# Kernel optimization log

Hardware: AMD Instinct MI355X
Metric: run time of the kernel (lower is better)

## Reference

```python
import jax, jax.numpy as jnp
import numpy as np

N, E = 10000, 320000
C_IN, C_OUT = 256, 128
EPS = 1e-5


def _p(key, shape, scale=0.02):
    return (jax.random.normal(key, shape, dtype=jnp.float32) * scale)


def setup_inputs() -> dict:
    key = jax.random.key(0)
    ks = jax.random.split(key, 16)
    inp = {
        "x": jax.random.normal(ks[0], (N, C_IN), dtype=jnp.float32),
        "edge_index": jax.random.randint(ks[1], (2, E), 0, N, dtype=jnp.int64),
        # GCNConv weights (stored [in, out] so forward is x @ W)
        "W1": _p(ks[2], (C_IN, C_OUT)), "b1": jnp.zeros((C_OUT,), jnp.float32),
        "W2": _p(ks[3], (C_OUT, C_OUT)), "b2": jnp.zeros((C_OUT,), jnp.float32),
        # LayerNorms
        "ln1_g": jnp.ones((C_OUT,), jnp.float32), "ln1_b": jnp.zeros((C_OUT,), jnp.float32),
        "ln2_g": jnp.ones((C_OUT,), jnp.float32), "ln2_b": jnp.zeros((C_OUT,), jnp.float32),
        # Attention QKV
        "Wq": _p(ks[4], (C_OUT, C_OUT)), "bq": jnp.zeros((C_OUT,), jnp.float32),
        "Wk": _p(ks[5], (C_OUT, C_OUT)), "bk": jnp.zeros((C_OUT,), jnp.float32),
        "Wv": _p(ks[6], (C_OUT, C_OUT)), "bv": jnp.zeros((C_OUT,), jnp.float32),
        # shortcut Linear (in_channels != out_channels)
        "Ws": _p(ks[7], (C_IN, C_OUT)), "bs": jnp.zeros((C_OUT,), jnp.float32),
    }
    return inp


def _gcn_conv(x, W, b, src, dst, n_nodes):
    # PyG GCNConv: h = x W; add self loops; sym-normalized scatter aggregation.
    h = x @ W  # [N, out]
    loop = jnp.arange(n_nodes, dtype=src.dtype)
    s = jnp.concatenate([src, loop])
    d = jnp.concatenate([dst, loop])
    deg = jax.ops.segment_sum(jnp.ones_like(d, dtype=h.dtype), d, num_segments=n_nodes)
    dis = jnp.where(deg > 0, jax.lax.rsqrt(deg), 0.0)  # deg^-1/2
    norm = dis[s] * dis[d]  # [E+N]
    agg = jax.ops.segment_sum(h[s] * norm[:, None], d, num_segments=n_nodes)
    return agg + b


def _layer_norm(x, g, b):
    mu = jnp.mean(x, axis=-1, keepdims=True)
    var = jnp.var(x, axis=-1, keepdims=True)
    return (x - mu) * jax.lax.rsqrt(var + EPS) * g + b


def reference(x, edge_index, W1, b1, W2, b2, ln1_g, ln1_b, ln2_g, ln2_b,
              Wq, bq, Wk, bk, Wv, bv, Ws, bs):
    src, dst = edge_index[0], edge_index[1]
    n = x.shape[0]
    identity = x @ Ws + bs
    out = _gcn_conv(x, W1, b1, src, dst, n)
    out = jax.nn.silu(_layer_norm(out, ln1_g, ln1_b))  # dropout = identity (eval)
    out = _gcn_conv(out, W2, b2, src, dst, n)
    out = _layer_norm(out, ln2_g, ln2_b)
    # dense self-attention over all nodes
    q = out @ Wq + bq
    k = out @ Wk + bk
    v = out @ Wv + bv
    scale = np.sqrt(out.shape[-1]).astype(np.float32)
    attn = jax.nn.softmax(q @ k.T / scale, axis=-1)  # [N, N]
    out = attn @ v + out
    return jax.nn.silu(out + identity)
```

## Files before the change

kernel.cpp:

```cpp
#include <hip/hip_runtime.h>
#include <hip/hip_bf16.h>

typedef unsigned short u16;
typedef unsigned int u32;
typedef __bf16 bf16x8 __attribute__((ext_vector_type(8)));
typedef float f32x4 __attribute__((ext_vector_type(4)));

#define MFMA16(a, b, c) __builtin_amdgcn_mfma_f32_16x16x32_bf16(a, b, c, 0, 0, 0)

static __device__ __forceinline__ u16 f2b(float f) {
  u32 u = __float_as_uint(f);
  return (u16)((u + 0x7FFFu + ((u >> 16) & 1u)) >> 16);
}
static __device__ __forceinline__ float blo(u32 u) { return __uint_as_float(u << 16); }
static __device__ __forceinline__ float bhi(u32 u) { return __uint_as_float(u & 0xffff0000u); }

static __device__ __forceinline__ void async_copy16(void* lds, const void* gp) {
  __builtin_amdgcn_global_load_lds(
      (const __attribute__((address_space(1))) unsigned int*)gp,
      (__attribute__((address_space(3))) unsigned int*)lds, 16, 0, 0);
}

__global__ void prep_kernel(const int* __restrict__ dst, int* __restrict__ degi, int E,
                            const float* __restrict__ x, u16* __restrict__ xb, int n4,
                            const float* __restrict__ W1, const float* __restrict__ Ws,
                            const float* __restrict__ W2, const float* __restrict__ Wq,
                            const float* __restrict__ Wk, const float* __restrict__ Wv,
                            u16* __restrict__ wout) {
  int t = blockIdx.x * 256 + threadIdx.x;
  if (t < E) { atomicAdd(&degi[dst[t]], 1); return; }
  int t2 = t - E;
  if (t2 < n4) {
    float4 v = *(const float4*)&x[t2 * 4];
    ushort4 o;
    o.x = f2b(v.x); o.y = f2b(v.y); o.z = f2b(v.z); o.w = f2b(v.w);
    *(ushort4*)&xb[t2 * 4] = o;
    return;
  }
  int u = t2 - n4;
  if (u >= 131072) return;
  const float* src; int K, base, loc;
  if (u < 65536) {
    if (u < 32768) { src = W1; base = 0; } else { src = Ws; base = 32768; }
    loc = u - base; K = 256;
  } else {
    int seg = (u - 65536) >> 14;
    src = (seg == 0) ? W2 : (seg == 1) ? Wq : (seg == 2) ? Wk : Wv;
    base = 65536 + seg * 16384; loc = u & 16383; K = 128;
  }
  int k = loc >> 7, c = loc & 127;
  wout[base + c * K + k] = f2b(src[loc]);
}

__global__ void dis_start_kernel(const int* __restrict__ degi, float* __restrict__ d,
                                 int* __restrict__ startb, int* __restrict__ counter, int N) {
  int i = blockIdx.x * 256 + threadIdx.x;
  int lane = threadIdx.x & 63;
  int dg = (i < N) ? degi[i] : 0;
  if (i < N) d[i] = rsqrtf((float)dg + 1.0f);
  int x = dg;
#pragma unroll
  for (int ofs = 1; ofs < 64; ofs <<= 1) {
    int y = __shfl_up(x, ofs, 64);
    if (lane >= ofs) x += y;
  }
  int waveTotal = __shfl(x, 63, 64);
  int base = 0;
  if (lane == 63) base = atomicAdd(counter, waveTotal);
  base = __shfl(base, 63, 64);
  if (i < N) startb[i] = base + x - dg;
}

__global__ void fill_kernel(const int* __restrict__ src, const int* __restrict__ dst,
                            const int* __restrict__ startb, int* __restrict__ cursor,
                            int* __restrict__ adj, int E) {
  int e = blockIdx.x * 256 + threadIdx.x;
  if (e < E) {
    int d = dst[e];
    int p = atomicAdd(&cursor[d], 1);
    adj[startb[d] + p] = src[e];
  }
}

__global__ __launch_bounds__(64) void bgemm_dual(
    const u16* __restrict__ A, const u16* __restrict__ Wa, const u16* __restrict__ Wb,
    const float* __restrict__ bsb, u16* __restrict__ outa, float* __restrict__ outb, int M)
{
  int lane = threadIdx.x;
  int col = lane & 15, quad = lane >> 4;
  int row0 = blockIdx.x * 16;
  int cb = blockIdx.y * 64;
  int ar = row0 + col; if (ar > M - 1) ar = M - 1;
  const u16* ap = A + (size_t)ar * 256 + quad * 8;
  f32x4 Oa[4], Ob[4];
#pragma unroll
  for (int i = 0; i < 4; i++) {
    Oa[i][0] = 0.f; Oa[i][1] = 0.f; Oa[i][2] = 0.f; Oa[i][3] = 0.f;
    Ob[i] = Oa[i];
  }
#pragma unroll
  for (int k0 = 0; k0 < 256; k0 += 32) {
    bf16x8 aA = *(const bf16x8*)(ap + k0);
#pragma unroll
    for (int nb = 0; nb < 4; nb++) {
      size_t wofs = (size_t)(cb + nb * 16 + col) * 256 + k0 + quad * 8;
      Oa[nb] = MFMA16(aA, *(const bf16x8*)(Wa + wofs), Oa[nb]);
      Ob[nb] = MFMA16(aA, *(const bf16x8*)(Wb + wofs), Ob[nb]);
    }
  }
#pragma unroll
  for (int nb = 0; nb < 4; nb++) {
    int ch = cb + nb * 16 + col;
    float bv = bsb[ch];
#pragma unroll
    for (int r = 0; r < 4; r++) {
      int row = row0 + quad * 4 + r;
      if (row >= M) continue;
      outa[(size_t)row * 128 + ch] = f2b(Oa[nb][r]);
      outb[(size_t)row * 128 + ch] = Ob[nb][r] + bv;
    }
  }
}

__global__ __launch_bounds__(64) void bgemm_single(
    const u16* __restrict__ A, const u16* __restrict__ Wt, u16* __restrict__ outa, int M)
{
  int lane = threadIdx.x;
  int col = lane & 15, quad = lane >> 4;
  int row0 = blockIdx.x * 16;
  int cb = blockIdx.y * 64;
  int ar = row0 + col; if (ar > M - 1) ar = M - 1;
  const u16* ap = A + (size_t)ar * 128 + quad * 8;
  f32x4 O[4];
#pragma unroll
  for (int i = 0; i < 4; i++) { O[i][0] = 0.f; O[i][1] = 0.f; O[i][2] = 0.f; O[i][3] = 0.f; }
#pragma unroll
  for (int k0 = 0; k0 < 128; k0 += 32) {
    bf16x8 aA = *(const bf16x8*)(ap + k0);
#pragma unroll
    for (int nb = 0; nb < 4; nb++) {
      O[nb] = MFMA16(aA, *(const bf16x8*)(Wt + (size_t)(cb + nb * 16 + col) * 128 + k0 + quad * 8), O[nb]);
    }
  }
#pragma unroll
  for (int nb = 0; nb < 4; nb++) {
    int ch = cb + nb * 16 + col;
#pragma unroll
    for (int r = 0; r < 4; r++) {
      int row = row0 + quad * 4 + r;
      if (row >= M) continue;
      outa[(size_t)row * 128 + ch] = f2b(O[nb][r]);
    }
  }
}

__global__ __launch_bounds__(64) void bgemm_qkv(
    const u16* __restrict__ A, const u16* __restrict__ Wqt, const u16* __restrict__ Wkt,
    const u16* __restrict__ Wvt, const float* __restrict__ bq, const float* __restrict__ bk,
    const float* __restrict__ bv, u16* __restrict__ q_out, u16* __restrict__ k_out,
    u16* __restrict__ v_out, int M, int NP, float qscale)
{
  int lane = threadIdx.x;
  int col = lane & 15, quad = lane >> 4;
  int row0 = blockIdx.x * 16;
  int cb = blockIdx.y * 64;
  int ar = row0 + col; if (ar > M - 1) ar = M - 1;
  const u16* ap = A + (size_t)ar * 128 + quad * 8;
  f32x4 Oq[4], Ok[4], Ov[4];
#pragma unroll
  for (int i = 0; i < 4; i++) {
    Oq[i][0] = 0.f; Oq[i][1] = 0.f; Oq[i][2] = 0.f; Oq[i][3] = 0.f;
    Ok[i] = Oq[i]; Ov[i] = Oq[i];
  }
#pragma unroll
  for (int k0 = 0; k0 < 128; k0 += 32) {
    bf16x8 aA = *(const bf16x8*)(ap + k0);
#pragma unroll
    for (int nb = 0; nb < 4; nb++) {
      size_t wofs = (size_t)(cb + nb * 16 + col) * 128 + k0 + quad * 8;
      Oq[nb] = MFMA16(aA, *(const bf16x8*)(Wqt + wofs), Oq[nb]);
      Ok[nb] = MFMA16(aA, *(const bf16x8*)(Wkt + wofs), Ok[nb]);
      Ov[nb] = MFMA16(aA, *(const bf16x8*)(Wvt + wofs), Ov[nb]);
    }
  }
#pragma unroll
  for (int nb = 0; nb < 4; nb++) {
    int ch = cb + nb * 16 + col;
    float bqv = bq[ch], bkv = bk[ch], bvv = bv[ch];
#pragma unroll
    for (int r = 0; r < 4; r++) {
      int row = row0 + quad * 4 + r;
      if (row >= M) continue;
      q_out[(size_t)row * 128 + ch] = f2b((Oq[nb][r] + bqv) * qscale);
      k_out[(size_t)row * 128 + ch] = f2b(Ok[nb][r] + bkv);
      v_out[(size_t)ch * NP + row] = f2b(Ov[nb][r] + bvv);
    }
  }
}

__global__ __launch_bounds__(256) void gather_ln(
    const u16* __restrict__ h, const float* __restrict__ dis,
    const int* __restrict__ adj, const int* __restrict__ startb, const int* __restrict__ degi,
    const float* __restrict__ bias, const float* __restrict__ g, const float* __restrict__ beta,
    float* __restrict__ out, u16* __restrict__ outb, int N, int do_silu)
{
  int row = blockIdx.x * 4 + (threadIdx.x >> 6);
  int lane = threadIdx.x & 63;
  if (row >= N) return;
  int st = startb[row], dg = degi[row];
  int c2 = lane * 2;
  float v0 = 0.f, v1 = 0.f;
  for (int base = 0; base < dg; base += 64) {
    int nb = min(64, dg - base);
    int myadj = 0; float mydis = 0.f;
    if (lane < nb) { myadj = adj[st + base + lane]; mydis = dis[myadj]; }
    int jj = 0;
    for (; jj + 8 <= nb; jj += 8) {
      int s0 = __shfl(myadj, jj),     s1 = __shfl(myadj, jj + 1);
      int s2 = __shfl(myadj, jj + 2), s3 = __shfl(myadj, jj + 3);
      int s4 = __shfl(myadj, jj + 4), s5 = __shfl(myadj, jj + 5);
      int s6 = __shfl(myadj, jj + 6), s7 = __shfl(myadj, jj + 7);
      float w0 = __shfl(mydis, jj),     w1 = __shfl(mydis, jj + 1);
      float w2 = __shfl(mydis, jj + 2), w3 = __shfl(mydis, jj + 3);
      float w4 = __shfl(mydis, jj + 4), w5 = __shfl(mydis, jj + 5);
      float w6 = __shfl(mydis, jj + 6), w7 = __shfl(mydis, jj + 7);
      u32 a0 = *(const u32*)&h[(size_t)s0 * 128 + c2];
      u32 a1 = *(const u32*)&h[(size_t)s1 * 128 + c2];
      u32 a2 = *(const u32*)&h[(size_t)s2 * 128 + c2];
      u32 a3 = *(const u32*)&h[(size_t)s3 * 128 + c2];
      u32 a4 = *(const u32*)&h[(size_t)s4 * 128 + c2];
      u32 a5 = *(const u32*)&h[(size_t)s5 * 128 + c2];
      u32 a6 = *(const u32*)&h[(size_t)s6 * 128 + c2];
      u32 a7 = *(const u32*)&h[(size_t)s7 * 128 + c2];
      v0 += w0 * blo(a0); v1 += w0 * bhi(a0);
      v0 += w1 * blo(a1); v1 += w1 * bhi(a1);
      v0 += w2 * blo(a2); v1 += w2 * bhi(a2);
      v0 += w3 * blo(a3); v1 += w3 * bhi(a3);
      v0 += w4 * blo(a4); v1 += w4 * bhi(a4);
      v0 += w5 * blo(a5); v1 += w5 * bhi(a5);
      v0 += w6 * blo(a6); v1 += w6 * bhi(a6);
      v0 += w7 * blo(a7); v1 += w7 * bhi(a7);
    }
    for (; jj < nb; jj++) {
      int s = __shfl(myadj, jj);
      float wv = __shfl(mydis, jj);
      u32 a = *(const u32*)&h[(size_t)s * 128 + c2];
      v0 += wv * blo(a); v1 += wv * bhi(a);
    }
  }
  float dd = dis[row];
  u32 aself = *(const u32*)&h[(size_t)row * 128 + c2];
  v0 = (v0 + dd * blo(aself)) * dd + bias[c2];
  v1 = (v1 + dd * bhi(aself)) * dd + bias[c2 + 1];
  float s = v0 + v1;
#pragma unroll
  for (int d = 32; d > 0; d >>= 1) s += __shfl_xor(s, d, 64);
  float mu = s * (1.0f / 128.0f);
  float d0 = v0 - mu, d1 = v1 - mu;
  float q = d0 * d0 + d1 * d1;
#pragma unroll
  for (int d = 32; d > 0; d >>= 1) q += __shfl_xor(q, d, 64);
  float rstd = rsqrtf(q * (1.0f / 128.0f) + 1e-5f);
  float o0 = d0 * rstd * g[c2]     + beta[c2];
  float o1 = d1 * rstd * g[c2 + 1] + beta[c2 + 1];
  if (do_silu) {
    o0 = o0 / (1.f + __expf(-o0));
    o1 = o1 / (1.f + __expf(-o1));
  }
  size_t base = (size_t)row * 128;
  *(float2*)&out[base + c2] = make_float2(o0, o1);
  u32 pk = (u32)f2b(o0) | ((u32)f2b(o1) << 16);
  *(u32*)&outb[base + c2] = pk;
}

__global__ __launch_bounds__(256, 3) void flash_part(
    const u16* __restrict__ qb, const u16* __restrict__ kb, const u16* __restrict__ vt,
    u16* __restrict__ Opart, float* __restrict__ lpart,
    int N, int NP, int CHUNK)
{
  __shared__ __align__(16) u16 Kl[2][32 * 128];
  __shared__ __align__(16) u16 Vl[2][128 * 32];
  __shared__ __align__(16) u16 Pl[4][32][40];
  int tid = threadIdx.x;
  int w = tid >> 6, lane = tid & 63;
  int col = lane & 15, quad = lane >> 4;
  int h8 = col & 7;
  int ks = blockIdx.y;
  int kstart = ks * CHUNK;
  int qbase = blockIdx.x * 128 + w * 32;

  bf16x8 aQ[2][4];
#pragma unroll
  for (int rg = 0; rg < 2; rg++) {
    int qr = qbase + rg * 16 + col; if (qr > N - 1) qr = N - 1;
    const u16* qp = qb + (size_t)qr * 128 + quad * 8;
    aQ[rg][0] = *(const bf16x8*)(qp);
    aQ[rg][1] = *(const bf16x8*)(qp + 32);
    aQ[rg][2] = *(const bf16x8*)(qp + 64);
    aQ[rg][3] = *(const bf16x8*)(qp + 96);
  }

  f32x4 O[2][8];
#pragma unroll
  for (int rg = 0; rg < 2; rg++)
#pragma unroll
    for (int i = 0; i < 8; i++) { O[rg][i][0] = 0.f; O[rg][i][1] = 0.f; O[rg][i][2] = 0.f; O[rg][i][3] = 0.f; }
  float lr[2][4] = {{0.f, 0.f, 0.f, 0.f}, {0.f, 0.f, 0.f, 0.f}};

  int l16 = lane >> 4, c16 = lane & 15;
  int vch = lane >> 2, vc4 = lane & 3;

  auto stage = [&](int buf, int k0) {
#pragma unroll
    for (int i = 0; i < 2; i++) {
      int rl = w * 8 + i * 4 + l16;
      int cg = c16 ^ (rl & 7);
      async_copy16(&Kl[buf][(w * 8 + i * 4) * 128], kb + (size_t)(k0 + rl) * 128 + cg * 8);
    }
#pragma unroll
    for (int i = 0; i < 2; i++) {
      int ch = w * 32 + i * 16 + vch;
      int cg = vc4 ^ ((ch >> 1) & 3);
      async_copy16(&Vl[buf][(w * 32 + i * 16) * 32], vt + (size_t)ch * NP + k0 + cg * 8);
    }
  };

  int KT = (min(CHUNK, NP - kstart)) >> 5;
  stage(0, kstart);

  for (int kt = 0; kt < KT; kt++) {
    int buf = kt & 1;
    int k0 = kstart + (kt << 5);
    asm volatile("s_waitcnt vmcnt(0)\n\ts_barrier" ::: "memory");
    if (kt + 1 < KT) stage(buf ^ 1, k0 + 32);

    const u16* Kb = &Kl[buf][0];
    const u16* Vb = &Vl[buf][0];
    bool edge = (k0 + 32 > N);
#pragma unroll
    for (int g = 0; g < 2; g++) {
      const u16* kr = Kb + (g * 16 + col) * 128;
      bf16x8 kf0 = *(const bf16x8*)(kr + (((0 + quad) ^ h8) << 3));
      bf16x8 kf1 = *(const bf16x8*)(kr + (((4 + quad) ^ h8) << 3));
      bf16x8 kf2 = *(const bf16x8*)(kr + (((8 + quad) ^ h8) << 3));
      bf16x8 kf3 = *(const bf16x8*)(kr + (((12 + quad) ^ h8) << 3));
      f32x4 s0; s0[0] = 0.f; s0[1] = 0.f; s0[2] = 0.f; s0[3] = 0.f;
      f32x4 s1 = s0;
      s0 = MFMA16(aQ[0][0], kf0, s0); s1 = MFMA16(aQ[1][0], kf0, s1);
      s0 = MFMA16(aQ[0][1], kf1, s0); s1 = MFMA16(aQ[1][1], kf1, s1);
      s0 = MFMA16(aQ[0][2], kf2, s0); s1 = MFMA16(aQ[1][2], kf2, s1);
      s0 = MFMA16(aQ[0][3], kf3, s0); s1 = MFMA16(aQ[1][3], kf3, s1);
      if (edge && (k0 + g * 16 + col >= N)) {
        s0[0] = -1e30f; s0[1] = -1e30f; s0[2] = -1e30f; s0[3] = -1e30f;
        s1 = s0;
      }
#pragma unroll
      for (int r = 0; r < 4; r++) {
        float p0 = __expf(s0[r]);
        float p1 = __expf(s1[r]);
        lr[0][r] += p0;
        lr[1][r] += p1;
        Pl[w][quad * 4 + r][g * 16 + col]      = (u16)(__float_as_uint(p0) >> 16);
        Pl[w][16 + quad * 4 + r][g * 16 + col] = (u16)(__float_as_uint(p1) >> 16);
      }
    }
    asm volatile("s_waitcnt lgkmcnt(0)" ::: "memory");
    bf16x8 aP0 = *(const bf16x8*)&Pl[w][col][quad * 8];
    bf16x8 aP1 = *(const bf16x8*)&Pl[w][16 + col][quad * 8];
#pragma unroll
    for (int nb = 0; nb < 8; nb++) {
      int ch = nb * 16 + col;
      const u16* vr = Vb + ch * 32;
      bf16x8 vf = *(const bf16x8*)(vr + ((quad ^ ((ch >> 1) & 3)) << 3));
      O[0][nb] = MFMA16(aP0, vf, O[0][nb]);
      O[1][nb] = MFMA16(aP1, vf, O[1][nb]);
    }
  }

#pragma unroll
  for (int d = 1; d < 16; d <<= 1) {
#pragma unroll
    for (int rg = 0; rg < 2; rg++)
#pragma unroll
      for (int r = 0; r < 4; r++) lr[rg][r] += __shfl_xor(lr[rg][r], d, 64);
  }

#pragma unroll
  for (int rg = 0; rg < 2; rg++) {
#pragma unroll
    for (int nb = 0; nb < 8; nb++) {
      int ch = nb * 16 + col;
#pragma unroll
      for (int r = 0; r < 4; r++) {
        int row = qbase + rg * 16 + quad * 4 + r;
        if (row < N)
          Opart[((size_t)ks * NP + row) * 128 + ch] = f2b(O[rg][nb][r]);
      }
    }
  }
  if (col == 0) {
#pragma unroll
    for (int rg = 0; rg < 2; rg++)
#pragma unroll
      for (int r = 0; r < 4; r++) {
        int row = qbase + rg * 16 + quad * 4 + r;
        if (row < N) lpart[(size_t)ks * NP + row] = lr[rg][r];
      }
  }
}

__global__ __launch_bounds__(256) void attn_combine(
    const u16* __restrict__ Opart, const float* __restrict__ lpart,
    const float* __restrict__ out2, const float* __restrict__ ident, float* __restrict__ out,
    int N, int NP, int S)
{
  int row = blockIdx.x * 4 + (threadIdx.x >> 6);
  int c2 = (threadIdx.x & 63) * 2;
  if (row >= N) return;
  float num0 = 0.f, num1 = 0.f, den = 0.f;
  for (int u = 0; u < S; u++) {
    u32 b = *(const u32*)&Opart[((size_t)u * NP + row) * 128 + c2];
    num0 += blo(b); num1 += bhi(b);
    den += lpart[(size_t)u * NP + row];
  }
  size_t idx = (size_t)row * 128 + c2;
  float rinv = 1.0f / den;
  float2 o2 = *(const float2*)&out2[idx];
  float2 id = *(const float2*)&ident[idx];
  float v0 = num0 * rinv + o2.x + id.x;
  float v1 = num1 * rinv + o2.y + id.y;
  v0 = v0 / (1.f + __expf(-v0));
  v1 = v1 / (1.f + __expf(-v1));
  *(float2*)&out[idx] = make_float2(v0, v1);
}

extern "C" void kernel_launch(void* const* d_in, const int* in_sizes, int n_in,
                              void* d_out, int out_size, void* d_ws, size_t ws_size,
                              hipStream_t stream) {
  const float* x   = (const float*)d_in[0];
  const int*   ei  = (const int*)d_in[1];
  const float* W1  = (const float*)d_in[2];
  const float* b1  = (const float*)d_in[3];
  const float* W2  = (const float*)d_in[4];
  const float* b2  = (const float*)d_in[5];
  const float* g1  = (const float*)d_in[6];
  const float* be1 = (const float*)d_in[7];
  const float* g2  = (const float*)d_in[8];
  const float* be2 = (const float*)d_in[9];
  const float* Wq  = (const float*)d_in[10];
  const float* bq  = (const float*)d_in[11];
  const float* Wk  = (const float*)d_in[12];
  const float* bk  = (const float*)d_in[13];
  const float* Wv  = (const float*)d_in[14];
  const float* bv  = (const float*)d_in[15];
  const float* Wsw = (const float*)d_in[16];
  const float* bs  = (const float*)d_in[17];

  const int CIN = 256, C = 128;
  int N = in_sizes[0] / CIN;
  int E = in_sizes[1] / 2;
  int NP = (N + 63) & ~63;
  const int* src = ei;
  const int* dstp = ei + E;

  const int S = 12;
  int tiles = NP / 64;
  int CHUNK = ((tiles + S - 1) / S) * 64;

  char* w = (char*)d_ws;
  size_t off = 0;
  auto alloc = [&](size_t bytes) -> void* {
    void* p = w + off;
    off = (off + bytes + 255) & ~(size_t)255;
    return p;
  };
  int*   degi   = (int*)alloc((size_t)N * 4);
  int*   cursor = (int*)alloc((size_t)N * 4);
  int*   counter= (int*)alloc(256);
  size_t zlen   = off;
  float* disb   = (float*)alloc((size_t)N * 4);
  int*   startb = (int*)alloc((size_t)N * 4);
  int*   adj    = (int*)alloc((size_t)E * 4);
  u16*   h      = (u16*)alloc((size_t)N * C * 2);
  float* ident  = (float*)alloc((size_t)N * C * 4);
  float* cur    = (float*)alloc((size_t)N * C * 4);
  u16*   xb     = (u16*)alloc((size_t)N * CIN * 2);
  u16*   curb   = (u16*)alloc((size_t)N * C * 2);
  u16*   wt     = (u16*)alloc((size_t)131072 * 2);
  u16*   qbb    = (u16*)alloc((size_t)N * C * 2);
  u16*   kbb    = (u16*)alloc((size_t)NP * C * 2);
  u16*   vt     = (u16*)alloc((size_t)C * NP * 2);
  u16*   Opart  = (u16*)alloc((size_t)S * NP * C * 2);
  float* lpart  = (float*)alloc((size_t)S * NP * 4);

  u16* wt1 = wt;
  u16* wts = wt + 32768;
  u16* wt2 = wt + 65536;
  u16* wtq = wt + 81920;
  u16* wtk = wt + 98304;
  u16* wtv = wt + 114688;

  hipMemsetAsync(degi, 0, zlen, stream);

  int n4 = N * CIN / 4;
  int ptot = E + n4 + 131072;
  prep_kernel<<<(ptot + 255) / 256, 256, 0, stream>>>(dstp, degi, E, x, xb, n4,
                                                      W1, Wsw, W2, Wq, Wk, Wv, wt);
  int gN = (N + 255) / 256, gE = (E + 255) / 256;
  dis_start_kernel<<<gN, 256, 0, stream>>>(degi, disb, startb, counter, N);
  fill_kernel<<<gE, 256, 0, stream>>>(src, dstp, startb, cursor, adj, E);

  dim3 gbg((N + 15) / 16, 2);
  bgemm_dual<<<gbg, 64, 0, stream>>>(xb, wt1, wts, bs, h, ident, N);
  gather_ln<<<(N + 3) / 4, 256, 0, stream>>>(h, disb, adj, startb, degi, b1, g1, be1, cur, curb, N, 1);
  bgemm_single<<<gbg, 64, 0, stream>>>(curb, wt2, h, N);
  gather_ln<<<(N + 3) / 4, 256, 0, stream>>>(h, disb, adj, startb, degi, b2, g2, be2, cur, curb, N, 0);

  const float qscale = 0.08838834764831845f;
  bgemm_qkv<<<gbg, 64, 0, stream>>>(curb, wtq, wtk, wtv, bq, bk, bv, qbb, kbb, vt, N, NP, qscale);

  dim3 fg((N + 127) / 128, S);
  flash_part<<<fg, 256, 0, stream>>>(qbb, kbb, vt, Opart, lpart, N, NP, CHUNK);
  attn_combine<<<(N + 3) / 4, 256, 0, stream>>>(Opart, lpart, cur, ident,
                                                (float*)d_out, N, NP, S);
}
```

Baseline: 295.8 us.

## Fuse gather+LayerNorm with following GEMMs and keep softmax probabilities in registers

Merges each graph-aggregation+LayerNorm pass with the next small GEMM (W2, and QKV) through an LDS tile, removing two kernel launches and the intermediate bf16 round trips. The flash attention kernel now computes S^T by swapping MFMA operands, so P can be moved between lanes with ds_bpermute instead of a per-wave LDS buffer. It also writes packed Opart rows and uses row sums reduced by cross-lane shuffles. The split count S drops from 12 to 8 and partial buffers are padded to 128 rows. Fused gather blocks now process 16 rows serially across 4 waves, which may reduce latency hiding in the gather phase.

Result: no change. 294.0 us (-0.6%).

```diff
diff --git a/kernel.cpp b/kernel.cpp
--- a/kernel.cpp
+++ b/kernel.cpp
@@ -14,6 +14,12 @@
 }
 static __device__ __forceinline__ float blo(u32 u) { return __uint_as_float(u << 16); }
 static __device__ __forceinline__ float bhi(u32 u) { return __uint_as_float(u & 0xffff0000u); }
+static __device__ __forceinline__ u32 packtrunc(float a, float b) {
+  return (__float_as_uint(a) >> 16) | (__float_as_uint(b) & 0xffff0000u);
+}
+static __device__ __forceinline__ bf16x8 mk8(u32 a, u32 b, u32 c, u32 d) {
+  union { u32 u[4]; bf16x8 v; } t; t.u[0] = a; t.u[1] = b; t.u[2] = c; t.u[3] = d; return t.v;
+}
 
 static __device__ __forceinline__ void async_copy16(void* lds, const void* gp) {
   __builtin_amdgcn_global_load_lds(
@@ -122,165 +128,177 @@
   }
 }
 
-__global__ __launch_bounds__(64) void bgemm_single(
-    const u16* __restrict__ A, const u16* __restrict__ Wt, u16* __restrict__ outa, int M)
-{
-  int lane = threadIdx.x;
-  int col = lane & 15, quad = lane >> 4;
-  int row0 = blockIdx.x * 16;
-  int cb = blockIdx.y * 64;
-  int ar = row0 + col; if (ar > M - 1) ar = M - 1;
-  const u16* ap = A + (size_t)ar * 128 + quad * 8;
-  f32x4 O[4];
-#pragma unroll
-  for (int i = 0; i < 4; i++) { O[i][0] = 0.f; O[i][1] = 0.f; O[i][2] = 0.f; O[i][3] = 0.f; }
-#pragma unroll
-  for (int k0 = 0; k0 < 128; k0 += 32) {
-    bf16x8 aA = *(const bf16x8*)(ap + k0);
-#pragma unroll
-    for (int nb = 0; nb < 4; nb++) {
-      O[nb] = MFMA16(aA, *(const bf16x8*)(Wt + (size_t)(cb + nb * 16 + col) * 128 + k0 + quad * 8), O[nb]);
-    }
-  }
-#pragma unroll
-  for (int nb = 0; nb < 4; nb++) {
-    int ch = cb + nb * 16 + col;
-#pragma unroll
-    for (int r = 0; r < 4; r++) {
-      int row = row0 + quad * 4 + r;
-      if (row >= M) continue;
-      outa[(size_t)row * 128 + ch] = f2b(O[nb][r]);
-    }
-  }
-}
-
-__global__ __launch_bounds__(64) void bgemm_qkv(
-    const u16* __restrict__ A, const u16* __restrict__ Wqt, const u16* __restrict__ Wkt,
-    const u16* __restrict__ Wvt, const float* __restrict__ bq, const float* __restrict__ bk,
-    const float* __restrict__ bv, u16* __restrict__ q_out, u16* __restrict__ k_out,
-    u16* __restrict__ v_out, int M, int NP, float qscale)
-{
-  int lane = threadIdx.x;
-  int col = lane & 15, quad = lane >> 4;
-  int row0 = blockIdx.x * 16;
-  int cb = blockIdx.y * 64;
-  int ar = row0 + col; if (ar > M - 1) ar = M - 1;
-  const u16* ap = A + (size_t)ar * 128 + quad * 8;
-  f32x4 Oq[4], Ok[4], Ov[4];
-#pragma unroll
-  for (int i = 0; i < 4; i++) {
-    Oq[i][0] = 0.f; Oq[i][1] = 0.f; Oq[i][2] = 0.f; Oq[i][3] = 0.f;
-    Ok[i] = Oq[i]; Ov[i] = Oq[i];
-  }
-#pragma unroll
-  for (int k0 = 0; k0 < 128; k0 += 32) {
-    bf16x8 aA = *(const bf16x8*)(ap + k0);
-#pragma unroll
-    for (int nb = 0; nb < 4; nb++) {
-      size_t wofs = (size_t)(cb + nb * 16 + col) * 128 + k0 + quad * 8;
-      Oq[nb] = MFMA16(aA, *(const bf16x8*)(Wqt + wofs), Oq[nb]);
-      Ok[nb] = MFMA16(aA, *(const bf16x8*)(Wkt + wofs), Ok[nb]);
-      Ov[nb] = MFMA16(aA, *(const bf16x8*)(Wvt + wofs), Ov[nb]);
-    }
-  }
-#pragma unroll
-  for (int nb = 0; nb < 4; nb++) {
-    int ch = cb + nb * 16 + col;
-    float bqv = bq[ch], bkv = bk[ch], bvv = bv[ch];
-#pragma unroll
-    for (int r = 0; r < 4; r++) {
-      int row = row0 + quad * 4 + r;
-      if (row >= M) continue;
-      q_out[(size_t)row * 128 + ch] = f2b((Oq[nb][r] + bqv) * qscale);
-      k_out[(size_t)row * 128 + ch] = f2b(Ok[nb][r] + bkv);
-      v_out[(size_t)ch * NP + row] = f2b(Ov[nb][r] + bvv);
-    }
-  }
-}
-
-__global__ __launch_bounds__(256) void gather_ln(
+static __device__ __forceinline__ void gather_rows_to_lds(
     const u16* __restrict__ h, const float* __restrict__ dis,
     const int* __restrict__ adj, const int* __restrict__ startb, const int* __restrict__ degi,
     const float* __restrict__ bias, const float* __restrict__ g, const float* __restrict__ beta,
-    float* __restrict__ out, u16* __restrict__ outb, int N, int do_silu)
+    u16* Ao, float* curOut, int row0, int N, int do_silu)
 {
-  int row = blockIdx.x * 4 + (threadIdx.x >> 6);
+  int w = threadIdx.x >> 6, lane = threadIdx.x & 63;
+  int c2 = lane * 2;
+  for (int rr = 0; rr < 4; rr++) {
+    int rl = w * 4 + rr;
+    int row = row0 + rl;
+    float o0 = 0.f, o1 = 0.f;
+    if (row < N) {
+      int st = startb[row], dg = degi[row];
+      float v0 = 0.f, v1 = 0.f;
+      for (int base = 0; base < dg; base += 64) {
+        int nb = min(64, dg - base);
+        int myadj = 0; float mydis = 0.f;
+        if (lane < nb) { myadj = adj[st + base + lane]; mydis = dis[myadj]; }
+        int jj = 0;
+        for (; jj + 8 <= nb; jj += 8) {
+          int s0 = __shfl(myadj, jj),     s1 = __shfl(myadj, jj + 1);
+          int s2 = __shfl(myadj, jj + 2), s3 = __shfl(myadj, jj + 3);
+          int s4 = __shfl(myadj, jj + 4), s5 = __shfl(myadj, jj + 5);
+          int s6 = __shfl(myadj, jj + 6), s7 = __shfl(myadj, jj + 7);
+          float w0 = __shfl(mydis, jj),     w1 = __shfl(mydis, jj + 1);
+          float w2 = __shfl(mydis, jj + 2), w3 = __shfl(mydis, jj + 3);
+          float w4 = __shfl(mydis, jj + 4), w5 = __shfl(mydis, jj + 5);
+          float w6 = __shfl(mydis, jj + 6), w7 = __shfl(mydis, jj + 7);
+          u32 a0 = *(const u32*)&h[(size_t)s0 * 128 + c2];
+          u32 a1 = *(const u32*)&h[(size_t)s1 * 128 + c2];
+          u32 a2 = *(const u32*)&h[(size_t)s2 * 128 + c2];
+          u32 a3 = *(const u32*)&h[(size_t)s3 * 128 + c2];
+          u32 a4 = *(const u32*)&h[(size_t)s4 * 128 + c2];
+          u32 a5 = *(const u32*)&h[(size_t)s5 * 128 + c2];
+          u32 a6 = *(const u32*)&h[(size_t)s6 * 128 + c2];
+          u32 a7 = *(const u32*)&h[(size_t)s7 * 128 + c2];
+          v0 += w0 * blo(a0); v1 += w0 * bhi(a0);
+          v0 += w1 * blo(a1); v1 += w1 * bhi(a1);
+          v0 += w2 * blo(a2); v1 += w2 * bhi(a2);
+          v0 += w3 * blo(a3); v1 += w3 * bhi(a3);
+          v0 += w4 * blo(a4); v1 += w4 * bhi(a4);
+          v0 += w5 * blo(a5); v1 += w5 * bhi(a5);
+          v0 += w6 * blo(a6); v1 += w6 * bhi(a6);
+          v0 += w7 * blo(a7); v1 += w7 * bhi(a7);
+        }
+        for (; jj < nb; jj++) {
+          int s = __shfl(myadj, jj);
+          float wv = __shfl(mydis, jj);
+          u32 a = *(const u32*)&h[(size_t)s * 128 + c2];
+          v0 += wv * blo(a); v1 += wv * bhi(a);
+        }
+      }
+      float dd = dis[row];
+      u32 aself = *(const u32*)&h[(size_t)row * 128 + c2];
+      v0 = (v0 + dd * blo(aself)) * dd + bias[c2];
+      v1 = (v1 + dd * bhi(aself)) * dd + bias[c2 + 1];
+      float s = v0 + v1;
+#pragma unroll
+      for (int d = 32; d > 0; d >>= 1) s += __shfl_xor(s, d, 64);
+      float mu = s * (1.0f / 128.0f);
+      float d0 = v0 - mu, d1 = v1 - mu;
+      float q = d0 * d0 + d1 * d1;
+#pragma unroll
+      for (int d = 32; d > 0; d >>= 1) q += __shfl_xor(q, d, 64);
+      float rstd = rsqrtf(q * (1.0f / 128.0f) + 1e-5f);
+      o0 = d0 * rstd * g[c2]     + beta[c2];
+      o1 = d1 * rstd * g[c2 + 1] + beta[c2 + 1];
+      if (do_silu) {
+        o0 = o0 / (1.f + __expf(-o0));
+        o1 = o1 / (1.f + __expf(-o1));
+      }
+      if (curOut) *(float2*)&curOut[(size_t)row * 128 + c2] = make_float2(o0, o1);
+    }
+    *(u32*)&Ao[rl * 136 + c2] = (u32)f2b(o0) | ((u32)f2b(o1) << 16);
+  }
+}
+
+__global__ __launch_bounds__(256) void gather_gemm1(
+    const u16* __restrict__ h, const float* __restrict__ dis,
+    const int* __restrict__ adj, const int* __restrict__ startb, const int* __restrict__ degi,
+    const float* __restrict__ b1, const float* __restrict__ g1, const float* __restrict__ be1,
+    const u16* __restrict__ W2t, u16* __restrict__ h2, int N)
+{
+  __shared__ __align__(16) u16 Ao[16 * 136];
+  int row0 = blockIdx.x * 16;
+  gather_rows_to_lds(h, dis, adj, startb, degi, b1, g1, be1, Ao, nullptr, row0, N, 1);
+  __syncthreads();
   int lane = threadIdx.x & 63;
-  if (row >= N) return;
-  int st = startb[row], dg = degi[row];
-  int c2 = lane * 2;
-  float v0 = 0.f, v1 = 0.f;
-  for (int base = 0; base < dg; base += 64) {
-    int nb = min(64, dg - base);
-    int myadj = 0; float mydis = 0.f;
-    if (lane < nb) { myadj = adj[st + base + lane]; mydis = dis[myadj]; }
-    int jj = 0;
-    for (; jj + 8 <= nb; jj += 8) {
-      int s0 = __shfl(myadj, jj),     s1 = __shfl(myadj, jj + 1);
-      int s2 = __shfl(myadj, jj + 2), s3 = __shfl(myadj, jj + 3);
-      int s4 = __shfl(myadj, jj + 4), s5 = __shfl(myadj, jj + 5);
-      int s6 = __shfl(myadj, jj + 6), s7 = __shfl(myadj, jj + 7);
-      float w0 = __shfl(mydis, jj),     w1 = __shfl(mydis, jj + 1);
-      float w2 = __shfl(mydis, jj + 2), w3 = __shfl(mydis, jj + 3);
-      float w4 = __shfl(mydis, jj + 4), w5 = __shfl(mydis, jj + 5);
-      float w6 = __shfl(mydis, jj + 6), w7 = __shfl(mydis, jj + 7);
-      u32 a0 = *(const u32*)&h[(size_t)s0 * 128 + c2];
-      u32 a1 = *(const u32*)&h[(size_t)s1 * 128 + c2];
-      u32 a2 = *(const u32*)&h[(size_t)s2 * 128 + c2];
-      u32 a3 = *(const u32*)&h[(size_t)s3 * 128 + c2];
-      u32 a4 = *(const u32*)&h[(size_t)s4 * 128 + c2];
-      u32 a5 = *(const u32*)&h[(size_t)s5 * 128 + c2];
-      u32 a6 = *(const u32*)&h[(size_t)s6 * 128 + c2];
-      u32 a7 = *(const u32*)&h[(size_t)s7 * 128 + c2];
-      v0 += w0 * blo(a0); v1 += w0 * bhi(a0);
-      v0 += w1 * blo(a1); v1 += w1 * bhi(a1);
-      v0 += w2 * blo(a2); v1 += w2 * bhi(a2);
-      v0 += w3 * blo(a3); v1 += w3 * bhi(a3);
-      v0 += w4 * blo(a4); v1 += w4 * bhi(a4);
-      v0 += w5 * blo(a5); v1 += w5 * bhi(a5);
-      v0 += w6 * blo(a6); v1 += w6 * bhi(a6);
-      v0 += w7 * blo(a7); v1 += w7 * bhi(a7);
-    }
-    for (; jj < nb; jj++) {
-      int s = __shfl(myadj, jj);
-      float wv = __shfl(mydis, jj);
-      u32 a = *(const u32*)&h[(size_t)s * 128 + c2];
-      v0 += wv * blo(a); v1 += wv * bhi(a);
-    }
-  }
-  float dd = dis[row];
-  u32 aself = *(const u32*)&h[(size_t)row * 128 + c2];
-  v0 = (v0 + dd * blo(aself)) * dd + bias[c2];
-  v1 = (v1 + dd * bhi(aself)) * dd + bias[c2 + 1];
-  float s = v0 + v1;
-#pragma unroll
-  for (int d = 32; d > 0; d >>= 1) s += __shfl_xor(s, d, 64);
-  float mu = s * (1.0f / 128.0f);
-  float d0 = v0 - mu, d1 = v1 - mu;
-  float q = d0 * d0 + d1 * d1;
-#pragma unroll
-  for (int d = 32; d > 0; d >>= 1) q += __shfl_xor(q, d, 64);
-  float rstd = rsqrtf(q * (1.0f / 128.0f) + 1e-5f);
-  float o0 = d0 * rstd * g[c2]     + beta[c2];
-  float o1 = d1 * rstd * g[c2 + 1] + beta[c2 + 1];
-  if (do_silu) {
-    o0 = o0 / (1.f + __expf(-o0));
-    o1 = o1 / (1.f + __expf(-o1));
-  }
-  size_t base = (size_t)row * 128;
-  *(float2*)&out[base + c2] = make_float2(o0, o1);
-  u32 pk = (u32)f2b(o0) | ((u32)f2b(o1) << 16);
-  *(u32*)&outb[base + c2] = pk;
+  int w = threadIdx.x >> 6;
+  int col = lane & 15, quad = lane >> 4;
+  int nb0 = w * 2;
+  f32x4 acc[2];
+#pragma unroll
+  for (int t = 0; t < 2; t++) { acc[t][0] = 0.f; acc[t][1] = 0.f; acc[t][2] = 0.f; acc[t][3] = 0.f; }
+#pragma unroll
+  for (int ks = 0; ks < 4; ks++) {
+    bf16x8 aA = *(const bf16x8*)&Ao[col * 136 + ks * 32 + quad * 8];
+#pragma unroll
+    for (int t = 0; t < 2; t++) {
+      const u16* bp = W2t + (size_t)((nb0 + t) * 16 + col) * 128 + ks * 32 + quad * 8;
+      acc[t] = MFMA16(aA, *(const bf16x8*)bp, acc[t]);
+    }
+  }
+#pragma unroll
+  for (int t = 0; t < 2; t++) {
+    int ch = (nb0 + t) * 16 + col;
+#pragma unroll
+    for (int r = 0; r < 4; r++) {
+      int row = row0 + quad * 4 + r;
+      if (row < N) h2[(size_t)row * 128 + ch] = f2b(acc[t][r]);
+    }
+  }
+}
+
+__global__ __launch_bounds__(256) void gather_gemm_qkv(
+    const u16* __restrict__ h2, const float* __restrict__ dis,
+    const int* __restrict__ adj, const int* __restrict__ startb, const int* __restrict__ degi,
+    const float* __restrict__ b2, const float* __restrict__ g2, const float* __restrict__ be2,
+    const u16* __restrict__ Wqt, const u16* __restrict__ Wkt, const u16* __restrict__ Wvt,
+    const float* __restrict__ bq, const float* __restrict__ bk, const float* __restrict__ bv,
+    float* __restrict__ cur, u16* __restrict__ q_out, u16* __restrict__ k_out,
+    u16* __restrict__ v_out, int N, int NP, float qscale)
+{
+  __shared__ __align__(16) u16 Ao[16 * 136];
+  int row0 = blockIdx.x * 16;
+  gather_rows_to_lds(h2, dis, adj, startb, degi, b2, g2, be2, Ao, cur, row0, N, 0);
+  __syncthreads();
+  int lane = threadIdx.x & 63;
+  int w = threadIdx.x >> 6;
+  int col = lane & 15, quad = lane >> 4;
+  int nb0 = w * 2;
+  f32x4 Oq[2], Ok[2], Ov[2];
+#pragma unroll
+  for (int t = 0; t < 2; t++) {
+    Oq[t][0] = 0.f; Oq[t][1] = 0.f; Oq[t][2] = 0.f; Oq[t][3] = 0.f;
+    Ok[t] = Oq[t]; Ov[t] = Oq[t];
+  }
+#pragma unroll
+  for (int ks = 0; ks < 4; ks++) {
+    bf16x8 aA = *(const bf16x8*)&Ao[col * 136 + ks * 32 + quad * 8];
+#pragma unroll
+    for (int t = 0; t < 2; t++) {
+      size_t wofs = (size_t)((nb0 + t) * 16 + col) * 128 + ks * 32 + quad * 8;
+      Oq[t] = MFMA16(aA, *(const bf16x8*)(Wqt + wofs), Oq[t]);
+      Ok[t] = MFMA16(aA, *(const bf16x8*)(Wkt + wofs), Ok[t]);
+      Ov[t] = MFMA16(aA, *(const bf16x8*)(Wvt + wofs), Ov[t]);
+    }
+  }
+#pragma unroll
+  for (int t = 0; t < 2; t++) {
+    int ch = (nb0 + t) * 16 + col;
+    float bqv = bq[ch], bkv = bk[ch], bvv = bv[ch];
+#pragma unroll
+    for (int r = 0; r < 4; r++) {
+      int row = row0 + quad * 4 + r;
+      if (row >= N) continue;
+      q_out[(size_t)row * 128 + ch] = f2b((Oq[t][r] + bqv) * qscale);
+      k_out[(size_t)row * 128 + ch] = f2b(Ok[t][r] + bkv);
+      v_out[(size_t)ch * NP + row] = f2b(Ov[t][r] + bvv);
+    }
+  }
 }
 
 __global__ __launch_bounds__(256, 3) void flash_part(
     const u16* __restrict__ qb, const u16* __restrict__ kb, const u16* __restrict__ vt,
     u16* __restrict__ Opart, float* __restrict__ lpart,
-    int N, int NP, int CHUNK)
+    int N, int NP, int NPB, int CHUNK)
 {
   __shared__ __align__(16) u16 Kl[2][32 * 128];
   __shared__ __align__(16) u16 Vl[2][128 * 32];
-  __shared__ __align__(16) u16 Pl[4][32][40];
   int tid = threadIdx.x;
   int w = tid >> 6, lane = tid & 63;
   int col = lane & 15, quad = lane >> 4;
@@ -305,10 +323,14 @@
   for (int rg = 0; rg < 2; rg++)
 #pragma unroll
     for (int i = 0; i < 8; i++) { O[rg][i][0] = 0.f; O[rg][i][1] = 0.f; O[rg][i][2] = 0.f; O[rg][i][3] = 0.f; }
-  float lr[2][4] = {{0.f, 0.f, 0.f, 0.f}, {0.f, 0.f, 0.f, 0.f}};
+  float lr0 = 0.f, lr1 = 0.f;
 
   int l16 = lane >> 4, c16 = lane & 15;
   int vch = lane >> 2, vc4 = lane & 3;
+
+  int idxA = (((quad & 1) * 2 + 0) * 16 + col) * 4;
+  int idxB = (((quad & 1) * 2 + 1) * 16 + col) * 4;
+  bool hiKg = (quad >= 2);
 
   auto stage = [&](int buf, int k0) {
 #pragma unroll
@@ -336,92 +358,104 @@
 
     const u16* Kb = &Kl[buf][0];
     const u16* Vb = &Vl[buf][0];
-    bool edge = (k0 + 32 > N);
-#pragma unroll
-    for (int g = 0; g < 2; g++) {
-      const u16* kr = Kb + (g * 16 + col) * 128;
+
+    f32x4 sT[2][2];
+#pragma unroll
+    for (int kg = 0; kg < 2; kg++) {
+      const u16* kr = Kb + (kg * 16 + col) * 128;
       bf16x8 kf0 = *(const bf16x8*)(kr + (((0 + quad) ^ h8) << 3));
       bf16x8 kf1 = *(const bf16x8*)(kr + (((4 + quad) ^ h8) << 3));
       bf16x8 kf2 = *(const bf16x8*)(kr + (((8 + quad) ^ h8) << 3));
       bf16x8 kf3 = *(const bf16x8*)(kr + (((12 + quad) ^ h8) << 3));
       f32x4 s0; s0[0] = 0.f; s0[1] = 0.f; s0[2] = 0.f; s0[3] = 0.f;
       f32x4 s1 = s0;
-      s0 = MFMA16(aQ[0][0], kf0, s0); s1 = MFMA16(aQ[1][0], kf0, s1);
-      s0 = MFMA16(aQ[0][1], kf1, s0); s1 = MFMA16(aQ[1][1], kf1, s1);
-      s0 = MFMA16(aQ[0][2], kf2, s0); s1 = MFMA16(aQ[1][2], kf2, s1);
-      s0 = MFMA16(aQ[0][3], kf3, s0); s1 = MFMA16(aQ[1][3], kf3, s1);
-      if (edge && (k0 + g * 16 + col >= N)) {
-        s0[0] = -1e30f; s0[1] = -1e30f; s0[2] = -1e30f; s0[3] = -1e30f;
-        s1 = s0;
+      s0 = MFMA16(kf0, aQ[0][0], s0); s1 = MFMA16(kf0, aQ[1][0], s1);
+      s0 = MFMA16(kf1, aQ[0][1], s0); s1 = MFMA16(kf1, aQ[1][1], s1);
+      s0 = MFMA16(kf2, aQ[0][2], s0); s1 = MFMA16(kf2, aQ[1][2], s1);
+      s0 = MFMA16(kf3, aQ[0][3], s0); s1 = MFMA16(kf3, aQ[1][3], s1);
+      sT[kg][0] = s0; sT[kg][1] = s1;
+    }
+    if (k0 + 32 > N) {
+#pragma unroll
+      for (int kg = 0; kg < 2; kg++) {
+        int kbase = k0 + kg * 16 + quad * 4;
+#pragma unroll
+        for (int r = 0; r < 4; r++) {
+          if (kbase + r >= N) { sT[kg][0][r] = -1e30f; sT[kg][1][r] = -1e30f; }
+        }
       }
-#pragma unroll
-      for (int r = 0; r < 4; r++) {
-        float p0 = __expf(s0[r]);
-        float p1 = __expf(s1[r]);
-        lr[0][r] += p0;
-        lr[1][r] += p1;
-        Pl[w][quad * 4 + r][g * 16 + col]      = (u16)(__float_as_uint(p0) >> 16);
-        Pl[w][16 + quad * 4 + r][g * 16 + col] = (u16)(__float_as_uint(p1) >> 16);
-      }
-    }
-    asm volatile("s_waitcnt lgkmcnt(0)" ::: "memory");
-    bf16x8 aP0 = *(const bf16x8*)&Pl[w][col][quad * 8];
-    bf16x8 aP1 = *(const bf16x8*)&Pl[w][16 + col][quad * 8];
+    }
+    u32 plo[2][2], phi[2][2];
+#pragma unroll
+    for (int kg = 0; kg < 2; kg++) {
+      float p00 = __expf(sT[kg][0][0]), p01 = __expf(sT[kg][0][1]);
+      float p02 = __expf(sT[kg][0][2]), p03 = __expf(sT[kg][0][3]);
+      float p10 = __expf(sT[kg][1][0]), p11 = __expf(sT[kg][1][1]);
+      float p12 = __expf(sT[kg][1][2]), p13 = __expf(sT[kg][1][3]);
+      lr0 += p00 + p01 + p02 + p03;
+      lr1 += p10 + p11 + p12 + p13;
+      plo[kg][0] = packtrunc(p00, p01); phi[kg][0] = packtrunc(p02, p03);
+      plo[kg][1] = packtrunc(p10, p11); phi[kg][1] = packtrunc(p12, p13);
+    }
+    bf16x8 bP[2];
+#pragma unroll
+    for (int rg = 0; rg < 2; rg++) {
+      int loA0 = __builtin_amdgcn_ds_bpermute(idxA, (int)plo[0][rg]);
+      int loA1 = __builtin_amdgcn_ds_bpermute(idxA, (int)plo[1][rg]);
+      int hiA0 = __builtin_amdgcn_ds_bpermute(idxA, (int)phi[0][rg]);
+      int hiA1 = __builtin_amdgcn_ds_bpermute(idxA, (int)phi[1][rg]);
+      int loB0 = __builtin_amdgcn_ds_bpermute(idxB, (int)plo[0][rg]);
+      int loB1 = __builtin_amdgcn_ds_bpermute(idxB, (int)plo[1][rg]);
+      int hiB0 = __builtin_amdgcn_ds_bpermute(idxB, (int)phi[0][rg]);
+      int hiB1 = __builtin_amdgcn_ds_bpermute(idxB, (int)phi[1][rg]);
+      u32 j01 = hiKg ? (u32)loA1 : (u32)loA0;
+      u32 j23 = hiKg ? (u32)hiA1 : (u32)hiA0;
+      u32 j45 = hiKg ? (u32)loB1 : (u32)loB0;
+      u32 j67 = hiKg ? (u32)hiB1 : (u32)hiB0;
+      bP[rg] = mk8(j01, j23, j45, j67);
+    }
 #pragma unroll
     for (int nb = 0; nb < 8; nb++) {
       int ch = nb * 16 + col;
       const u16* vr = Vb + ch * 32;
       bf16x8 vf = *(const bf16x8*)(vr + ((quad ^ ((ch >> 1) & 3)) << 3));
-      O[0][nb] = MFMA16(aP0, vf, O[0][nb]);
-      O[1][nb] = MFMA16(aP1, vf, O[1][nb]);
-    }
-  }
-
-#pragma unroll
-  for (int d = 1; d < 16; d <<= 1) {
-#pragma unroll
-    for (int rg = 0; rg < 2; rg++)
-#pragma unroll
-      for (int r = 0; r < 4; r++) lr[rg][r] += __shfl_xor(lr[rg][r], d, 64);
-  }
-
+      O[0][nb] = MFMA16(vf, bP[0], O[0][nb]);
+      O[1][nb] = MFMA16(vf, bP[1], O[1][nb]);
+    }
+  }
+
+  lr0 += __shfl_xor(lr0, 16, 64); lr0 += __shfl_xor(lr0, 32, 64);
+  lr1 += __shfl_xor(lr1, 16, 64); lr1 += __shfl_xor(lr1, 32, 64);
+  if (lane < 16) {
+    lpart[(size_t)ks * NPB + qbase + lane] = lr0;
+    lpart[(size_t)ks * NPB + qbase + 16 + lane] = lr1;
+  }
 #pragma unroll
   for (int rg = 0; rg < 2; rg++) {
+    int row = qbase + rg * 16 + col;
+    u16* dstrow = Opart + ((size_t)ks * NPB + row) * 128 + quad * 4;
 #pragma unroll
     for (int nb = 0; nb < 8; nb++) {
-      int ch = nb * 16 + col;
-#pragma unroll
-      for (int r = 0; r < 4; r++) {
-        int row = qbase + rg * 16 + quad * 4 + r;
-        if (row < N)
-          Opart[((size_t)ks * NP + row) * 128 + ch] = f2b(O[rg][nb][r]);
-      }
-    }
-  }
-  if (col == 0) {
-#pragma unroll
-    for (int rg = 0; rg < 2; rg++)
-#pragma unroll
-      for (int r = 0; r < 4; r++) {
-        int row = qbase + rg * 16 + quad * 4 + r;
-        if (row < N) lpart[(size_t)ks * NP + row] = lr[rg][r];
-      }
+      u32 w01 = (u32)f2b(O[rg][nb][0]) | ((u32)f2b(O[rg][nb][1]) << 16);
+      u32 w23 = (u32)f2b(O[rg][nb][2]) | ((u32)f2b(O[rg][nb][3]) << 16);
+      *(uint2*)(dstrow + nb * 16) = make_uint2(w01, w23);
+    }
   }
 }
 
 __global__ __launch_bounds__(256) void attn_combine(
     const u16* __restrict__ Opart, const float* __restrict__ lpart,
     const float* __restrict__ out2, const float* __restrict__ ident, float* __restrict__ out,
-    int N, int NP, int S)
+    int N, int NPB, int S)
 {
   int row = blockIdx.x * 4 + (threadIdx.x >> 6);
   int c2 = (threadIdx.x & 63) * 2;
   if (row >= N) return;
   float num0 = 0.f, num1 = 0.f, den = 0.f;
   for (int u = 0; u < S; u++) {
-    u32 b = *(const u32*)&Opart[((size_t)u * NP + row) * 128 + c2];
+    u32 b = *(const u32*)&Opart[((size_t)u * NPB + row) * 128 + c2];
     num0 += blo(b); num1 += bhi(b);
-    den += lpart[(size_t)u * NP + row];
+    den += lpart[(size_t)u * NPB + row];
   }
   size_t idx = (size_t)row * 128 + c2;
   float rinv = 1.0f / den;
@@ -460,10 +494,11 @@
   int N = in_sizes[0] / CIN;
   int E = in_sizes[1] / 2;
   int NP = (N + 63) & ~63;
+  int NPB = (N + 127) & ~127;
   const int* src = ei;
   const int* dstp = ei + E;
 
-  const int S = 12;
+  const int S = 8;
   int tiles = NP / 64;
   int CHUNK = ((tiles + S - 1) / S) * 64;
 
@@ -482,16 +517,16 @@
   int*   startb = (int*)alloc((size_t)N * 4);
   int*   adj    = (int*)alloc((size_t)E * 4);
   u16*   h      = (u16*)alloc((size_t)N * C * 2);
+  u16*   h2     = (u16*)alloc((size_t)N * C * 2);
   float* ident  = (float*)alloc((size_t)N * C * 4);
   float* cur    = (float*)alloc((size_t)N * C * 4);
   u16*   xb     = (u16*)alloc((size_t)N * CIN * 2);
-  u16*   curb   = (u16*)alloc((size_t)N * C * 2);
   u16*   wt     = (u16*)alloc((size_t)131072 * 2);
   u16*   qbb    = (u16*)alloc((size_t)N * C * 2);
   u16*   kbb    = (u16*)alloc((size_t)NP * C * 2);
   u16*   vt     = (u16*)alloc((size_t)C * NP * 2);
-  u16*   Opart  = (u16*)alloc((size_t)S * NP * C * 2);
-  float* lpart  = (float*)alloc((size_t)S * NP * 4);
+  u16*   Opart  = (u16*)alloc((size_t)S * NPB * C * 2);
+  float* lpart  = (float*)alloc((size_t)S * NPB * 4);
 
   u16* wt1 = wt;
   u16* wts = wt + 32768;
@@ -512,15 +547,17 @@
 
   dim3 gbg((N + 15) / 16, 2);
   bgemm_dual<<<gbg, 64, 0, stream>>>(xb, wt1, wts, bs, h, ident, N);
-  gather_ln<<<(N + 3) / 4, 256, 0, stream>>>(h, disb, adj, startb, degi, b1, g1, be1, cur, curb, N, 1);
-  bgemm_single<<<gbg, 64, 0, stream>>>(curb, wt2, h, N);
-  gather_ln<<<(N + 3) / 4, 256, 0, stream>>>(h, disb, adj, startb, degi, b2, g2, be2, cur, curb, N, 0);
+
+  int gRows = (N + 15) / 16;
+  gather_gemm1<<<gRows, 256, 0, stream>>>(h, disb, adj, startb, degi, b1, g1, be1, wt2, h2, N);
 
   const float qscale = 0.08838834764831845f;
-  bgemm_qkv<<<gbg, 64, 0, stream>>>(curb, wtq, wtk, wtv, bq, bk, bv, qbb, kbb, vt, N, NP, qscale);
-
-  dim3 fg((N + 127) / 128, S);
-  flash_part<<<fg, 256, 0, stream>>>(qbb, kbb, vt, Opart, lpart, N, NP, CHUNK);
+  gather_gemm_qkv<<<gRows, 256, 0, stream>>>(h2, disb, adj, startb, degi, b2, g2, be2,
+                                             wtq, wtk, wtv, bq, bk, bv,
+                                             cur, qbb, kbb, vt, N, NP, qscale);
+
+  dim3 fg(NPB / 128, S);
+  flash_part<<<fg, 256, 0, stream>>>(qbb, kbb, vt, Opart, lpart, N, NP, NPB, CHUNK);
   attn_combine<<<(N + 3) / 4, 256, 0, stream>>>(Opart, lpart, cur, ident,
-                                                (float*)d_out, N, NP, S);
-}
+                                                (float*)d_out, N, NPB, S);
+}
```
